# Kernel optimization log

Hardware: AMD Instinct MI355X
Metric: run time of the kernel (lower is better)

Reference implementation:

```python
import jax, jax.numpy as jnp
import numpy as np

B, S, D, H, DH, CACHE = 2, 2048, 1024, 16, 64, 2048
MAX_KV = 4096
F16_MAX = 65504.0  # tf.float16.max, used as the additive mask penalty in the original


def setup_inputs() -> dict:
    key = jax.random.key(0)
    ks = jax.random.split(key, 9)
    s = 0.02
    return {
        "q": jax.random.normal(ks[0], (B, S, D), jnp.float32),
        "k": jax.random.normal(ks[1], (B, S, D), jnp.float32),
        "v": jax.random.normal(ks[2], (B, S, D), jnp.float32),
        "cache_k": jax.random.normal(ks[3], (B, 1, CACHE, DH), jnp.float32),
        "cache_v": jax.random.normal(ks[4], (B, 1, CACHE, DH), jnp.float32),
        "wq": jax.random.normal(ks[5], (D, H * DH), jnp.float32) * s,
        "wk": jax.random.normal(ks[6], (D, DH), jnp.float32) * s,
        "wv": jax.random.normal(ks[7], (D, DH), jnp.float32) * s,
        "wo": jax.random.normal(ks[8], (H * DH, D), jnp.float32) * s,
    }


def reference(q, k, v, cache_k, cache_v, wq, wk, wv, wo):
    scale = 1.0 / np.sqrt(DH).astype(np.float32)
    b, s = q.shape[0], q.shape[1]
    # projections
    qh = (q @ wq).reshape(b, s, H, DH).transpose(0, 2, 1, 3)        # [B,H,S,dh]
    kh = (k @ wk).reshape(b, s, 1, DH).transpose(0, 2, 1, 3)        # [B,1,S,dh]
    vh = (v @ wv).reshape(b, s, 1, DH).transpose(0, 2, 1, 3)        # [B,1,S,dh]
    # KV cache concat + truncate to max_kv_length
    kc = jnp.concatenate([cache_k, kh], axis=2)[:, :, -MAX_KV:, :]  # [B,1,K,dh]
    vc = jnp.concatenate([cache_v, vh], axis=2)[:, :, -MAX_KV:, :]
    kk = kc[:, 0]  # [B,K,dh]  (single shared KV head)
    vv = vc[:, 0]
    # scores: [B,H,S,K]
    scores = jnp.einsum("bhqd,bkd->bhqk", qh, kk) * scale
    # causal mask exactly as tf.linalg.band_part(ones, -1, 0): mask[i,j] = j <= i
    klen = kk.shape[1]
    causal = jnp.tril(jnp.ones((s, klen), bool))                    # [S,K]
    scores = scores - (1.0 - causal.astype(scores.dtype)) * F16_MAX
    att = jax.nn.softmax(scores, axis=-1)
    vals = jnp.einsum("bhqk,bkd->bhqd", att, vv)                    # [B,H,S,dh]
    vals = vals.transpose(0, 2, 1, 3).reshape(b, s, H * DH)
    out = vals @ wo                                                 # [B,S,D]
    return out, kc, vc
```

## Files before the change

### kernel.cpp

```cpp
#include <hip/hip_runtime.h>
#include <hip/hip_bf16.h>
#include <type_traits>

#define B_ 2
#define S_ 2048
#define D_ 1024
#define H_ 16
#define DH_ 64
#define CACHE_ 2048
#define MAXKV_ 4096

using f32x4  = __attribute__((ext_vector_type(4))) float;
using bf16x8 = __attribute__((ext_vector_type(8))) short;
using bf16x4 = __attribute__((ext_vector_type(4))) short;

__device__ inline short f2bf(float x) {
  __hip_bfloat16 h = __float2bfloat16(x);
  short r;
  __builtin_memcpy(&r, &h, 2);
  return r;
}
__device__ inline void stor(float* p, float x) { *p = x; }
__device__ inline void stor(__hip_bfloat16* p, float x) { *p = __float2bfloat16(x); }

__device__ inline void glds16(const short* g, short* l) {
  __builtin_amdgcn_global_load_lds(
      (const __attribute__((address_space(1))) void*)g,
      (__attribute__((address_space(3))) void*)l, 16, 0, 0);
}

__device__ inline void tile_transpose(const float* __restrict__ in,
                                      short* __restrict__ out, int R, int C,
                                      int r0, int c0, int t, float T[64][65]) {
#pragma unroll
  for (int p = 0; p < 16; ++p) {
    int li = t + p * 256;
    int r = li >> 6, c = li & 63;
    T[r][c] = in[(size_t)(r0 + r) * C + c0 + c];
  }
  __syncthreads();
#pragma unroll
  for (int p = 0; p < 16; ++p) {
    int li = t + p * 256;
    int c = li >> 6, r = li & 63;
    out[(size_t)(c0 + c) * R + r0 + r] = f2bf(T[r][c]);
  }
}

__global__ __launch_bounds__(256) void prep_kernel(
    const float* __restrict__ q, const float* __restrict__ ck,
    const float* __restrict__ cv, const float* __restrict__ wq,
    const float* __restrict__ wk, const float* __restrict__ wv,
    const float* __restrict__ wo, short* __restrict__ qbf,
    float4* __restrict__ kc, float4* __restrict__ vc,
    short* __restrict__ ckbf, short* __restrict__ cvT,
    short* __restrict__ wqT, short* __restrict__ wkT,
    short* __restrict__ wvT, short* __restrict__ woT) {
  __shared__ float T[64][65];
  const int bx = blockIdx.x, t = threadIdx.x;
  if (bx < 1024) {
    int base = bx * 4096 + t * 4;
#pragma unroll
    for (int p = 0; p < 4; ++p) {
      int i = base + p * 1024;
      float4 f = *(const float4*)&q[i];
      bf16x4 s;
      s[0] = f2bf(f.x); s[1] = f2bf(f.y); s[2] = f2bf(f.z); s[3] = f2bf(f.w);
      *(bf16x4*)&qbf[i] = s;
    }
  } else if (bx < 1280) {
    int idx = (bx - 1024) * 256 + t;
    const int per_b = CACHE_ * DH_ / 4;
    int b = idx / per_b, rem = idx % per_b;
    int dst = b * (MAXKV_ * DH_ / 4) + rem;
    float4 a = ((const float4*)ck)[idx], c = ((const float4*)cv)[idx];
    kc[dst] = a;
    vc[dst] = c;
    bf16x4 s;
    s[0] = f2bf(a.x); s[1] = f2bf(a.y); s[2] = f2bf(a.z); s[3] = f2bf(a.w);
    *(bf16x4*)&ckbf[idx * 4] = s;
  } else if (bx < 1344) {
    int tt = bx - 1280;
    int b = tt >> 5, tile = tt & 31;
    tile_transpose(cv + (size_t)b * CACHE_ * DH_, cvT + (size_t)b * DH_ * CACHE_,
                   CACHE_, DH_, tile * 64, 0, t, T);
  } else if (bx < 1856) {
    int tt = bx - 1344;
    int sel = tt >> 8;
    tt &= 255;
    tile_transpose(sel ? wo : wq, sel ? woT : wqT, D_, D_, (tt >> 4) * 64,
                   (tt & 15) * 64, t, T);
  } else {
    int tt = bx - 1856;
    int sel = tt >> 4, tile = tt & 15;
    tile_transpose(sel ? wv : wk, sel ? wvT : wkT, D_, DH_, tile * 64, 0, t, T);
  }
}

__global__ __launch_bounds__(256) void gemm_kv(
    const float* __restrict__ A, const short* __restrict__ Bt,
    float* __restrict__ C, int K, const float* __restrict__ A2,
    const short* __restrict__ Bt2, float* __restrict__ C2) {
  if (blockIdx.z) { A = A2; Bt = Bt2; C = C2; }
  __shared__ __align__(16) short As[64 * 40];
  __shared__ __align__(16) short Bs[64 * 40];
  const int t = threadIdx.x;
  const int w = t >> 6, lane = t & 63, lx = lane & 15, quad = lane >> 4;
  const int row_base = (w >> 1) * 32, col_base = (w & 1) * 32;
  const int row0 = blockIdx.x * 64;

  f32x4 acc[2][2];
#pragma unroll
  for (int mb = 0; mb < 2; ++mb)
#pragma unroll
    for (int cb = 0; cb < 2; ++cb) acc[mb][cb] = (f32x4){0.f, 0.f, 0.f, 0.f};

  for (int k0 = 0; k0 < K; k0 += 32) {
#pragma unroll
    for (int p = 0; p < 2; ++p) {
      int li = t + p * 256;
      int row = li >> 3, kk0 = (li & 7) * 4;
      float4 f = *(const float4*)&A[(size_t)(row0 + row) * K + k0 + kk0];
      bf16x4 s;
      s[0] = f2bf(f.x); s[1] = f2bf(f.y); s[2] = f2bf(f.z); s[3] = f2bf(f.w);
      *(bf16x4*)&As[row * 40 + kk0] = s;
    }
    {
      int row = t >> 2, kk0 = (t & 3) * 8;
      *(bf16x8*)&Bs[row * 40 + kk0] =
          *(const bf16x8*)&Bt[(size_t)row * K + k0 + kk0];
    }
    __syncthreads();
    bf16x8 a[2], b[2];
#pragma unroll
    for (int mb = 0; mb < 2; ++mb)
      a[mb] = *(bf16x8*)&As[(row_base + mb * 16 + lx) * 40 + quad * 8];
#pragma unroll
    for (int cb = 0; cb < 2; ++cb)
      b[cb] = *(bf16x8*)&Bs[(col_base + cb * 16 + lx) * 40 + quad * 8];
#pragma unroll
    for (int mb = 0; mb < 2; ++mb)
#pragma unroll
      for (int cb = 0; cb < 2; ++cb)
        acc[mb][cb] = __builtin_amdgcn_mfma_f32_16x16x32_bf16(
            a[mb], b[cb], acc[mb][cb], 0, 0, 0);
    __syncthreads();
  }

#pragma unroll
  for (int mb = 0; mb < 2; ++mb)
#pragma unroll
    for (int cb = 0; cb < 2; ++cb)
#pragma unroll
      for (int reg = 0; reg < 4; ++reg) {
        int r = row0 + row_base + mb * 16 + quad * 4 + reg;
        int c = col_base + cb * 16 + lx;
        int bb = r >> 11, s = r & 2047;
        C[(size_t)bb * (MAXKV_ * DH_) + (size_t)(CACHE_ + s) * DH_ + c] =
            acc[mb][cb][reg];
      }
}

template <typename TC>
__global__ __launch_bounds__(256) void gemm_glds(
    const short* __restrict__ A, const short* __restrict__ Bt,
    TC* __restrict__ C, int M, int N, int K, float scale) {
  __shared__ __align__(16) short As[128 * 32];
  __shared__ __align__(16) short Bs[128 * 32];
  const int t = threadIdx.x;
  const int w = t >> 6, lane = t & 63, lx = lane & 15, quad = lane >> 4;
  const int row0 = blockIdx.x * 128, col0 = blockIdx.y * 128;
  const int row_base = (w >> 1) * 64, col_base = (w & 1) * 64;

  const short* Ag = A + (size_t)(row0 + w * 32 + (lane >> 2)) * K + (lane & 3) * 8;
  const short* Bg = Bt + (size_t)(col0 + w * 32 + (lane >> 2)) * K + (lane & 3) * 8;
  short* Al = &As[(w * 32) * 32];
  short* Bl = &Bs[(w * 32) * 32];

  f32x4 acc[4][4];
#pragma unroll
  for (int mb = 0; mb < 4; ++mb)
#pragma unroll
    for (int cb = 0; cb < 4; ++cb) acc[mb][cb] = (f32x4){0.f, 0.f, 0.f, 0.f};

  for (int k0 = 0; k0 < K; k0 += 32) {
    glds16(Ag + k0, Al);
    glds16(Ag + 16 * K + k0, Al + 16 * 32);
    glds16(Bg + k0, Bl);
    glds16(Bg + 16 * K + k0, Bl + 16 * 32);
    __syncthreads();
    bf16x8 a[4], b[4];
#pragma unroll
    for (int mb = 0; mb < 4; ++mb)
      a[mb] = *(bf16x8*)&As[(row_base + mb * 16 + lx) * 32 + quad * 8];
#pragma unroll
    for (int cb = 0; cb < 4; ++cb)
      b[cb] = *(bf16x8*)&Bs[(col_base + cb * 16 + lx) * 32 + quad * 8];
#pragma unroll
    for (int mb = 0; mb < 4; ++mb)
#pragma unroll
      for (int cb = 0; cb < 4; ++cb)
        acc[mb][cb] = __builtin_amdgcn_mfma_f32_16x16x32_bf16(
            a[mb], b[cb], acc[mb][cb], 0, 0, 0);
    __syncthreads();
  }

#pragma unroll
  for (int mb = 0; mb < 4; ++mb)
#pragma unroll
    for (int cb = 0; cb < 4; ++cb)
#pragma unroll
      for (int reg = 0; reg < 4; ++reg) {
        int r = row0 + row_base + mb * 16 + quad * 4 + reg;
        int c = col0 + col_base + cb * 16 + lx;
        stor(&C[(size_t)r * N + c], acc[mb][cb][reg] * scale);
      }
}

__global__ __launch_bounds__(256) void attention_mfma(
    __hip_bfloat16* __restrict__ qh,
    const short* __restrict__ ckbf,
    const short* __restrict__ cvT) {
  __shared__ __align__(16) short Ks[64 * 72];
  __shared__ __align__(16) short Vt[64 * 72];
  __shared__ __align__(16) short Ps[64 * 72];
  const int t = threadIdx.x;
  const int w = t >> 6, lane = t & 63, lx = lane & 15, quad = lane >> 4;
  const int p = blockIdx.x, bh = blockIdx.y;
  const int b = bh >> 4, h = bh & 15;
  const int qtA = p, qtB = 31 - p;
  const int q0A = qtA * 64, q0B = qtB * 64;
  short* qhp = (short*)qh;

  bf16x8 aqA[2], aqB[2];
#pragma unroll
  for (int kb = 0; kb < 2; ++kb) {
    aqA[kb] = *(const bf16x8*)&qhp[(size_t)(b * S_ + q0A + w * 16 + lx) * (H_ * DH_) +
                                   h * DH_ + kb * 32 + quad * 8];
    aqB[kb] = *(const bf16x8*)&qhp[(size_t)(b * S_ + q0B + w * 16 + lx) * (H_ * DH_) +
                                   h * DH_ + kb * 32 + quad * 8];
  }

  f32x4 oA[4], oB[4];
#pragma unroll
  for (int d = 0; d < 4; ++d) {
    oA[d] = (f32x4){0.f, 0.f, 0.f, 0.f};
    oB[d] = (f32x4){0.f, 0.f, 0.f, 0.f};
  }
  float lA[4] = {0.f, 0.f, 0.f, 0.f}, lB[4] = {0.f, 0.f, 0.f, 0.f};

  for (int kt = 0; kt <= qtB; ++kt) {
    const int k0 = kt * 64;
#pragma unroll
    for (int pp = 0; pp < 2; ++pp) {
      int li = t + pp * 256;
      int row = li >> 3, kk0 = (li & 7) * 8;
      *(bf16x8*)&Ks[row * 72 + kk0] =
          *(const bf16x8*)&ckbf[(size_t)(b * CACHE_ + k0 + row) * DH_ + kk0];
      *(bf16x8*)&Vt[row * 72 + kk0] =
          *(const bf16x8*)&cvT[(size_t)(b * DH_ + row) * CACHE_ + k0 + kk0];
    }
    __syncthreads();

    {
      f32x4 accs[4];
#pragma unroll
      for (int cb = 0; cb < 4; ++cb) accs[cb] = (f32x4){0.f, 0.f, 0.f, 0.f};
#pragma unroll
      for (int cb = 0; cb < 4; ++cb)
#pragma unroll
        for (int kb = 0; kb < 2; ++kb) {
          bf16x8 bk = *(bf16x8*)&Ks[(cb * 16 + lx) * 72 + kb * 32 + quad * 8];
          accs[cb] = __builtin_amdgcn_mfma_f32_16x16x32_bf16(aqB[kb], bk, accs[cb], 0, 0, 0);
        }
      const bool diag = (kt == qtB);
#pragma unroll
      for (int cb = 0; cb < 4; ++cb)
#pragma unroll
        for (int reg = 0; reg < 4; ++reg) {
          float x = accs[cb][reg];
          if (diag && (cb * 16 + lx > w * 16 + quad * 4 + reg)) x = -1e30f;
          float pe = __expf(x - 10.0f);
          Ps[(w * 16 + quad * 4 + reg) * 72 + cb * 16 + lx] = f2bf(pe);
          lB[reg] += pe;
        }
#pragma unroll
      for (int kb = 0; kb < 2; ++kb) {
        bf16x8 ap = *(bf16x8*)&Ps[(w * 16 + lx) * 72 + kb * 32 + quad * 8];
#pragma unroll
        for (int d = 0; d < 4; ++d) {
          bf16x8 bv = *(bf16x8*)&Vt[(d * 16 + lx) * 72 + kb * 32 + quad * 8];
          oB[d] = __builtin_amdgcn_mfma_f32_16x16x32_bf16(ap, bv, oB[d], 0, 0, 0);
        }
      }
    }

    if (kt <= qtA) {
      f32x4 accs[4];
#pragma unroll
      for (int cb = 0; cb < 4; ++cb) accs[cb] = (f32x4){0.f, 0.f, 0.f, 0.f};
#pragma unroll
      for (int cb = 0; cb < 4; ++cb)
#pragma unroll
        for (int kb = 0; kb < 2; ++kb) {
          bf16x8 bk = *(bf16x8*)&Ks[(cb * 16 + lx) * 72 + kb * 32 + quad * 8];
          accs[cb] = __builtin_amdgcn_mfma_f32_16x16x32_bf16(aqA[kb], bk, accs[cb], 0, 0, 0);
        }
      const bool diag = (kt == qtA);
#pragma unroll
      for (int cb = 0; cb < 4; ++cb)
#pragma unroll
        for (int reg = 0; reg < 4; ++reg) {
          float x = accs[cb][reg];
          if (diag && (cb * 16 + lx > w * 16 + quad * 4 + reg)) x = -1e30f;
          float pe = __expf(x - 10.0f);
          Ps[(w * 16 + quad * 4 + reg) * 72 + cb * 16 + lx] = f2bf(pe);
          lA[reg] += pe;
        }
#pragma unroll
      for (int kb = 0; kb < 2; ++kb) {
        bf16x8 ap = *(bf16x8*)&Ps[(w * 16 + lx) * 72 + kb * 32 + quad * 8];
#pragma unroll
        for (int d = 0; d < 4; ++d) {
          bf16x8 bv = *(bf16x8*)&Vt[(d * 16 + lx) * 72 + kb * 32 + quad * 8];
          oA[d] = __builtin_amdgcn_mfma_f32_16x16x32_bf16(ap, bv, oA[d], 0, 0, 0);
        }
      }
    }
    __syncthreads();
  }

#pragma unroll
  for (int off = 1; off < 16; off <<= 1)
#pragma unroll
    for (int reg = 0; reg < 4; ++reg) {
      lA[reg] += __shfl_xor(lA[reg], off, 64);
      lB[reg] += __shfl_xor(lB[reg], off, 64);
    }

#pragma unroll
  for (int d = 0; d < 4; ++d)
#pragma unroll
    for (int reg = 0; reg < 4; ++reg) {
      int col = h * DH_ + d * 16 + lx;
      int qA = q0A + w * 16 + quad * 4 + reg;
      int qB = q0B + w * 16 + quad * 4 + reg;
      qhp[(size_t)(b * S_ + qA) * (H_ * DH_) + col] = f2bf(oA[d][reg] / lA[reg]);
      qhp[(size_t)(b * S_ + qB) * (H_ * DH_) + col] = f2bf(oB[d][reg] / lB[reg]);
    }
}

extern "C" void kernel_launch(void* const* d_in, const int* in_sizes, int n_in,
                              void* d_out, int out_size, void* d_ws, size_t ws_size,
                              hipStream_t stream) {
  const float* q  = (const float*)d_in[0];
  const float* k  = (const float*)d_in[1];
  const float* v  = (const float*)d_in[2];
  const float* ck = (const float*)d_in[3];
  const float* cv = (const float*)d_in[4];
  const float* wq = (const float*)d_in[5];
  const float* wk = (const float*)d_in[6];
  const float* wv = (const float*)d_in[7];
  const float* wo = (const float*)d_in[8];

  float* out = (float*)d_out;
  float* kc  = out + (size_t)B_ * S_ * D_;
  float* vc  = kc + (size_t)B_ * MAXKV_ * DH_;

  short* qbf = (short*)d_out;

  short* ws   = (short*)d_ws;
  short* qh   = ws;
  short* ckbf = qh + (size_t)B_ * S_ * H_ * DH_;
  short* cvT  = ckbf + (size_t)B_ * CACHE_ * DH_;
  short* wqT  = cvT + (size_t)B_ * CACHE_ * DH_;
  short* wkT  = wqT + (size_t)D_ * H_ * DH_;
  short* wvT  = wkT + (size_t)D_ * DH_;
  short* woT  = wvT + (size_t)D_ * DH_;

  prep_kernel<<<1888, 256, 0, stream>>>(q, ck, cv, wq, wk, wv, wo, qbf,
                                        (float4*)kc, (float4*)vc, ckbf, cvT,
                                        wqT, wkT, wvT, woT);
  gemm_kv<<<dim3(64, 1, 2), 256, 0, stream>>>(k, wkT, kc, D_, v, wvT, vc);
  gemm_glds<__hip_bfloat16><<<dim3(32, 8), 256, 0, stream>>>(
      qbf, wqT, (__hip_bfloat16*)qh, B_ * S_, H_ * DH_, D_, 0.125f);
  attention_mfma<<<dim3(16, B_ * H_), 256, 0, stream>>>(
      (__hip_bfloat16*)qh, ckbf, cvT);
  gemm_glds<float><<<dim3(32, 8), 256, 0, stream>>>(
      qh, woT, out, B_ * S_, D_, D_, 1.0f);
}
```

Measured before the change: 231.4 us.

## Shrink GEMM tiles per wave, interleave dual-tile attention with transposed MFMA

The K/V projection GEMM now uses 32-row blocks, doubling the grid. The Q/O projection GEMMs run 512 threads per block, so each wave owns a 32x64 sub-tile instead of 64x64, giving more waves and fewer registers per wave. The attention kernel computes the transposed score product so each lane holds one query row. That makes the row-sum a single scalar and allows vectorized bf16x4 writes of P and of the output. It also interleaves the MFMAs for the two query tiles, using separate P buffers. The trade-off is more blocks and less reuse of each shared-memory load in the GEMMs, in exchange for better latency hiding and fewer scattered stores.

```diff
diff --git a/kernel.cpp b/kernel.cpp
--- a/kernel.cpp
+++ b/kernel.cpp
@@ -102,24 +102,20 @@
     float* __restrict__ C, int K, const float* __restrict__ A2,
     const short* __restrict__ Bt2, float* __restrict__ C2) {
   if (blockIdx.z) { A = A2; Bt = Bt2; C = C2; }
-  __shared__ __align__(16) short As[64 * 40];
+  __shared__ __align__(16) short As[32 * 40];
   __shared__ __align__(16) short Bs[64 * 40];
   const int t = threadIdx.x;
   const int w = t >> 6, lane = t & 63, lx = lane & 15, quad = lane >> 4;
-  const int row_base = (w >> 1) * 32, col_base = (w & 1) * 32;
-  const int row0 = blockIdx.x * 64;
-
-  f32x4 acc[2][2];
-#pragma unroll
-  for (int mb = 0; mb < 2; ++mb)
-#pragma unroll
-    for (int cb = 0; cb < 2; ++cb) acc[mb][cb] = (f32x4){0.f, 0.f, 0.f, 0.f};
+  const int row_base = (w & 1) * 16, col_base = (w >> 1) * 32;
+  const int row0 = blockIdx.x * 32;
+
+  f32x4 acc[2];
+  acc[0] = (f32x4){0.f, 0.f, 0.f, 0.f};
+  acc[1] = (f32x4){0.f, 0.f, 0.f, 0.f};
 
   for (int k0 = 0; k0 < K; k0 += 32) {
-#pragma unroll
-    for (int p = 0; p < 2; ++p) {
-      int li = t + p * 256;
-      int row = li >> 3, kk0 = (li & 7) * 4;
+    {
+      int row = t >> 3, kk0 = (t & 7) * 4;
       float4 f = *(const float4*)&A[(size_t)(row0 + row) * K + k0 + kk0];
       bf16x4 s;
       s[0] = f2bf(f.x); s[1] = f2bf(f.y); s[2] = f2bf(f.z); s[3] = f2bf(f.w);
@@ -131,38 +127,29 @@
           *(const bf16x8*)&Bt[(size_t)row * K + k0 + kk0];
     }
     __syncthreads();
-    bf16x8 a[2], b[2];
-#pragma unroll
-    for (int mb = 0; mb < 2; ++mb)
-      a[mb] = *(bf16x8*)&As[(row_base + mb * 16 + lx) * 40 + quad * 8];
-#pragma unroll
-    for (int cb = 0; cb < 2; ++cb)
-      b[cb] = *(bf16x8*)&Bs[(col_base + cb * 16 + lx) * 40 + quad * 8];
-#pragma unroll
-    for (int mb = 0; mb < 2; ++mb)
-#pragma unroll
-      for (int cb = 0; cb < 2; ++cb)
-        acc[mb][cb] = __builtin_amdgcn_mfma_f32_16x16x32_bf16(
-            a[mb], b[cb], acc[mb][cb], 0, 0, 0);
-    __syncthreads();
-  }
-
-#pragma unroll
-  for (int mb = 0; mb < 2; ++mb)
-#pragma unroll
-    for (int cb = 0; cb < 2; ++cb)
-#pragma unroll
-      for (int reg = 0; reg < 4; ++reg) {
-        int r = row0 + row_base + mb * 16 + quad * 4 + reg;
-        int c = col_base + cb * 16 + lx;
-        int bb = r >> 11, s = r & 2047;
-        C[(size_t)bb * (MAXKV_ * DH_) + (size_t)(CACHE_ + s) * DH_ + c] =
-            acc[mb][cb][reg];
-      }
+    bf16x8 a = *(bf16x8*)&As[(row_base + lx) * 40 + quad * 8];
+#pragma unroll
+    for (int cb = 0; cb < 2; ++cb) {
+      bf16x8 b = *(bf16x8*)&Bs[(col_base + cb * 16 + lx) * 40 + quad * 8];
+      acc[cb] = __builtin_amdgcn_mfma_f32_16x16x32_bf16(a, b, acc[cb], 0, 0, 0);
+    }
+    __syncthreads();
+  }
+
+#pragma unroll
+  for (int cb = 0; cb < 2; ++cb)
+#pragma unroll
+    for (int reg = 0; reg < 4; ++reg) {
+      int r = row0 + row_base + quad * 4 + reg;
+      int c = col_base + cb * 16 + lx;
+      int bb = r >> 11, s = r & 2047;
+      C[(size_t)bb * (MAXKV_ * DH_) + (size_t)(CACHE_ + s) * DH_ + c] =
+          acc[cb][reg];
+    }
 }
 
 template <typename TC>
-__global__ __launch_bounds__(256) void gemm_glds(
+__global__ __launch_bounds__(512) void gemm_glds(
     const short* __restrict__ A, const short* __restrict__ Bt,
     TC* __restrict__ C, int M, int N, int K, float scale) {
   __shared__ __align__(16) short As[128 * 32];
@@ -170,34 +157,32 @@
   const int t = threadIdx.x;
   const int w = t >> 6, lane = t & 63, lx = lane & 15, quad = lane >> 4;
   const int row0 = blockIdx.x * 128, col0 = blockIdx.y * 128;
-  const int row_base = (w >> 1) * 64, col_base = (w & 1) * 64;
-
-  const short* Ag = A + (size_t)(row0 + w * 32 + (lane >> 2)) * K + (lane & 3) * 8;
-  const short* Bg = Bt + (size_t)(col0 + w * 32 + (lane >> 2)) * K + (lane & 3) * 8;
-  short* Al = &As[(w * 32) * 32];
-  short* Bl = &Bs[(w * 32) * 32];
-
-  f32x4 acc[4][4];
-#pragma unroll
-  for (int mb = 0; mb < 4; ++mb)
+  const int row_base = (w >> 1) * 32, col_base = (w & 1) * 64;
+
+  const short* Ag = A + (size_t)(row0 + w * 16 + (lane >> 2)) * K + (lane & 3) * 8;
+  const short* Bg = Bt + (size_t)(col0 + w * 16 + (lane >> 2)) * K + (lane & 3) * 8;
+  short* Al = &As[(w * 16) * 32];
+  short* Bl = &Bs[(w * 16) * 32];
+
+  f32x4 acc[2][4];
+#pragma unroll
+  for (int mb = 0; mb < 2; ++mb)
 #pragma unroll
     for (int cb = 0; cb < 4; ++cb) acc[mb][cb] = (f32x4){0.f, 0.f, 0.f, 0.f};
 
   for (int k0 = 0; k0 < K; k0 += 32) {
     glds16(Ag + k0, Al);
-    glds16(Ag + 16 * K + k0, Al + 16 * 32);
     glds16(Bg + k0, Bl);
-    glds16(Bg + 16 * K + k0, Bl + 16 * 32);
-    __syncthreads();
-    bf16x8 a[4], b[4];
-#pragma unroll
-    for (int mb = 0; mb < 4; ++mb)
+    __syncthreads();
+    bf16x8 a[2], b[4];
+#pragma unroll
+    for (int mb = 0; mb < 2; ++mb)
       a[mb] = *(bf16x8*)&As[(row_base + mb * 16 + lx) * 32 + quad * 8];
 #pragma unroll
     for (int cb = 0; cb < 4; ++cb)
       b[cb] = *(bf16x8*)&Bs[(col_base + cb * 16 + lx) * 32 + quad * 8];
 #pragma unroll
-    for (int mb = 0; mb < 4; ++mb)
+    for (int mb = 0; mb < 2; ++mb)
 #pragma unroll
       for (int cb = 0; cb < 4; ++cb)
         acc[mb][cb] = __builtin_amdgcn_mfma_f32_16x16x32_bf16(
@@ -206,7 +191,7 @@
   }
 
 #pragma unroll
-  for (int mb = 0; mb < 4; ++mb)
+  for (int mb = 0; mb < 2; ++mb)
 #pragma unroll
     for (int cb = 0; cb < 4; ++cb)
 #pragma unroll
@@ -223,21 +208,23 @@
     const short* __restrict__ cvT) {
   __shared__ __align__(16) short Ks[64 * 72];
   __shared__ __align__(16) short Vt[64 * 72];
-  __shared__ __align__(16) short Ps[64 * 72];
+  __shared__ __align__(16) short PsA[64 * 72];
+  __shared__ __align__(16) short PsB[64 * 72];
   const int t = threadIdx.x;
   const int w = t >> 6, lane = t & 63, lx = lane & 15, quad = lane >> 4;
   const int p = blockIdx.x, bh = blockIdx.y;
   const int b = bh >> 4, h = bh & 15;
   const int qtA = p, qtB = 31 - p;
   const int q0A = qtA * 64, q0B = qtB * 64;
+  const int qrow = w * 16 + lx;
   short* qhp = (short*)qh;
 
   bf16x8 aqA[2], aqB[2];
 #pragma unroll
   for (int kb = 0; kb < 2; ++kb) {
-    aqA[kb] = *(const bf16x8*)&qhp[(size_t)(b * S_ + q0A + w * 16 + lx) * (H_ * DH_) +
+    aqA[kb] = *(const bf16x8*)&qhp[(size_t)(b * S_ + q0A + qrow) * (H_ * DH_) +
                                    h * DH_ + kb * 32 + quad * 8];
-    aqB[kb] = *(const bf16x8*)&qhp[(size_t)(b * S_ + q0B + w * 16 + lx) * (H_ * DH_) +
+    aqB[kb] = *(const bf16x8*)&qhp[(size_t)(b * S_ + q0B + qrow) * (H_ * DH_) +
                                    h * DH_ + kb * 32 + quad * 8];
   }
 
@@ -247,7 +234,7 @@
     oA[d] = (f32x4){0.f, 0.f, 0.f, 0.f};
     oB[d] = (f32x4){0.f, 0.f, 0.f, 0.f};
   }
-  float lA[4] = {0.f, 0.f, 0.f, 0.f}, lB[4] = {0.f, 0.f, 0.f, 0.f};
+  float lA = 0.f, lB = 0.f;
 
   for (int kt = 0; kt <= qtB; ++kt) {
     const int k0 = kt * 64;
@@ -262,92 +249,91 @@
     }
     __syncthreads();
 
+    const bool actA = (kt <= qtA);
+
+    f32x4 sA[4], sB[4];
+#pragma unroll
+    for (int cb = 0; cb < 4; ++cb) {
+      sA[cb] = (f32x4){0.f, 0.f, 0.f, 0.f};
+      sB[cb] = (f32x4){0.f, 0.f, 0.f, 0.f};
+    }
+#pragma unroll
+    for (int cb = 0; cb < 4; ++cb)
+#pragma unroll
+      for (int kb = 0; kb < 2; ++kb) {
+        bf16x8 kf = *(bf16x8*)&Ks[(cb * 16 + lx) * 72 + kb * 32 + quad * 8];
+        sB[cb] = __builtin_amdgcn_mfma_f32_16x16x32_bf16(kf, aqB[kb], sB[cb], 0, 0, 0);
+        if (actA)
+          sA[cb] = __builtin_amdgcn_mfma_f32_16x16x32_bf16(kf, aqA[kb], sA[cb], 0, 0, 0);
+      }
+
     {
-      f32x4 accs[4];
-#pragma unroll
-      for (int cb = 0; cb < 4; ++cb) accs[cb] = (f32x4){0.f, 0.f, 0.f, 0.f};
-#pragma unroll
-      for (int cb = 0; cb < 4; ++cb)
-#pragma unroll
-        for (int kb = 0; kb < 2; ++kb) {
-          bf16x8 bk = *(bf16x8*)&Ks[(cb * 16 + lx) * 72 + kb * 32 + quad * 8];
-          accs[cb] = __builtin_amdgcn_mfma_f32_16x16x32_bf16(aqB[kb], bk, accs[cb], 0, 0, 0);
+      const bool diag = (kt == qtB);
+#pragma unroll
+      for (int cb = 0; cb < 4; ++cb) {
+        bf16x4 pk;
+#pragma unroll
+        for (int reg = 0; reg < 4; ++reg) {
+          float x = sB[cb][reg];
+          if (diag && (cb * 16 + quad * 4 + reg > qrow)) x = -1e30f;
+          float pe = __expf(x - 10.0f);
+          lB += pe;
+          pk[reg] = f2bf(pe);
         }
-      const bool diag = (kt == qtB);
-#pragma unroll
-      for (int cb = 0; cb < 4; ++cb)
+        *(bf16x4*)&PsB[qrow * 72 + cb * 16 + quad * 4] = pk;
+      }
+    }
+    if (actA) {
+      const bool diag = (kt == qtA);
+#pragma unroll
+      for (int cb = 0; cb < 4; ++cb) {
+        bf16x4 pk;
 #pragma unroll
         for (int reg = 0; reg < 4; ++reg) {
-          float x = accs[cb][reg];
-          if (diag && (cb * 16 + lx > w * 16 + quad * 4 + reg)) x = -1e30f;
+          float x = sA[cb][reg];
+          if (diag && (cb * 16 + quad * 4 + reg > qrow)) x = -1e30f;
           float pe = __expf(x - 10.0f);
-          Ps[(w * 16 + quad * 4 + reg) * 72 + cb * 16 + lx] = f2bf(pe);
-          lB[reg] += pe;
+          lA += pe;
+          pk[reg] = f2bf(pe);
         }
-#pragma unroll
-      for (int kb = 0; kb < 2; ++kb) {
-        bf16x8 ap = *(bf16x8*)&Ps[(w * 16 + lx) * 72 + kb * 32 + quad * 8];
-#pragma unroll
-        for (int d = 0; d < 4; ++d) {
-          bf16x8 bv = *(bf16x8*)&Vt[(d * 16 + lx) * 72 + kb * 32 + quad * 8];
-          oB[d] = __builtin_amdgcn_mfma_f32_16x16x32_bf16(ap, bv, oB[d], 0, 0, 0);
-        }
-      }
-    }
-
-    if (kt <= qtA) {
-      f32x4 accs[4];
-#pragma unroll
-      for (int cb = 0; cb < 4; ++cb) accs[cb] = (f32x4){0.f, 0.f, 0.f, 0.f};
-#pragma unroll
-      for (int cb = 0; cb < 4; ++cb)
-#pragma unroll
-        for (int kb = 0; kb < 2; ++kb) {
-          bf16x8 bk = *(bf16x8*)&Ks[(cb * 16 + lx) * 72 + kb * 32 + quad * 8];
-          accs[cb] = __builtin_amdgcn_mfma_f32_16x16x32_bf16(aqA[kb], bk, accs[cb], 0, 0, 0);
-        }
-      const bool diag = (kt == qtA);
-#pragma unroll
-      for (int cb = 0; cb < 4; ++cb)
-#pragma unroll
-        for (int reg = 0; reg < 4; ++reg) {
-          float x = accs[cb][reg];
-          if (diag && (cb * 16 + lx > w * 16 + quad * 4 + reg)) x = -1e30f;
-          float pe = __expf(x - 10.0f);
-          Ps[(w * 16 + quad * 4 + reg) * 72 + cb * 16 + lx] = f2bf(pe);
-          lA[reg] += pe;
-        }
-#pragma unroll
-      for (int kb = 0; kb < 2; ++kb) {
-        bf16x8 ap = *(bf16x8*)&Ps[(w * 16 + lx) * 72 + kb * 32 + quad * 8];
-#pragma unroll
-        for (int d = 0; d < 4; ++d) {
-          bf16x8 bv = *(bf16x8*)&Vt[(d * 16 + lx) * 72 + kb * 32 + quad * 8];
-          oA[d] = __builtin_amdgcn_mfma_f32_16x16x32_bf16(ap, bv, oA[d], 0, 0, 0);
-        }
-      }
-    }
-    __syncthreads();
-  }
-
-#pragma unroll
-  for (int off = 1; off < 16; off <<= 1)
+        *(bf16x4*)&PsA[qrow * 72 + cb * 16 + quad * 4] = pk;
+      }
+    }
+
+#pragma unroll
+    for (int kb = 0; kb < 2; ++kb) {
+      bf16x8 pB = *(bf16x8*)&PsB[qrow * 72 + kb * 32 + quad * 8];
+      bf16x8 pA;
+      if (actA) pA = *(bf16x8*)&PsA[qrow * 72 + kb * 32 + quad * 8];
+#pragma unroll
+      for (int dcb = 0; dcb < 4; ++dcb) {
+        bf16x8 vf = *(bf16x8*)&Vt[(dcb * 16 + lx) * 72 + kb * 32 + quad * 8];
+        oB[dcb] = __builtin_amdgcn_mfma_f32_16x16x32_bf16(vf, pB, oB[dcb], 0, 0, 0);
+        if (actA)
+          oA[dcb] = __builtin_amdgcn_mfma_f32_16x16x32_bf16(vf, pA, oA[dcb], 0, 0, 0);
+      }
+    }
+    __syncthreads();
+  }
+
+  lA += __shfl_xor(lA, 16, 64);
+  lA += __shfl_xor(lA, 32, 64);
+  lB += __shfl_xor(lB, 16, 64);
+  lB += __shfl_xor(lB, 32, 64);
+  float iA = 1.f / lA, iB = 1.f / lB;
+
+#pragma unroll
+  for (int dcb = 0; dcb < 4; ++dcb) {
+    bf16x4 pa, pb;
 #pragma unroll
     for (int reg = 0; reg < 4; ++reg) {
-      lA[reg] += __shfl_xor(lA[reg], off, 64);
-      lB[reg] += __shfl_xor(lB[reg], off, 64);
-    }
-
-#pragma unroll
-  for (int d = 0; d < 4; ++d)
-#pragma unroll
-    for (int reg = 0; reg < 4; ++reg) {
-      int col = h * DH_ + d * 16 + lx;
-      int qA = q0A + w * 16 + quad * 4 + reg;
-      int qB = q0B + w * 16 + quad * 4 + reg;
-      qhp[(size_t)(b * S_ + qA) * (H_ * DH_) + col] = f2bf(oA[d][reg] / lA[reg]);
-      qhp[(size_t)(b * S_ + qB) * (H_ * DH_) + col] = f2bf(oB[d][reg] / lB[reg]);
-    }
+      pa[reg] = f2bf(oA[dcb][reg] * iA);
+      pb[reg] = f2bf(oB[dcb][reg] * iB);
+    }
+    size_t col = h * DH_ + dcb * 16 + quad * 4;
+    *(bf16x4*)&qhp[(size_t)(b * S_ + q0A + qrow) * (H_ * DH_) + col] = pa;
+    *(bf16x4*)&qhp[(size_t)(b * S_ + q0B + qrow) * (H_ * DH_) + col] = pb;
+  }
 }
 
 extern "C" void kernel_launch(void* const* d_in, const int* in_sizes, int n_in,
@@ -381,11 +367,11 @@
   prep_kernel<<<1888, 256, 0, stream>>>(q, ck, cv, wq, wk, wv, wo, qbf,
                                         (float4*)kc, (float4*)vc, ckbf, cvT,
                                         wqT, wkT, wvT, woT);
-  gemm_kv<<<dim3(64, 1, 2), 256, 0, stream>>>(k, wkT, kc, D_, v, wvT, vc);
-  gemm_glds<__hip_bfloat16><<<dim3(32, 8), 256, 0, stream>>>(
+  gemm_kv<<<dim3(128, 1, 2), 256, 0, stream>>>(k, wkT, kc, D_, v, wvT, vc);
+  gemm_glds<__hip_bfloat16><<<dim3(32, 8), 512, 0, stream>>>(
       qbf, wqT, (__hip_bfloat16*)qh, B_ * S_, H_ * DH_, D_, 0.125f);
   attention_mfma<<<dim3(16, B_ * H_), 256, 0, stream>>>(
       (__hip_bfloat16*)qh, ckbf, cvT);
-  gemm_glds<float><<<dim3(32, 8), 256, 0, stream>>>(
+  gemm_glds<float><<<dim3(32, 8), 512, 0, stream>>>(
       qh, woT, out, B_ * S_, D_, D_, 1.0f);
 }
```

Measured after the change: 252.1 us. 8.9% more time.
